# Kernel optimization log

Measured on AMD Instinct MI355X. Metric: run time of the kernel, lower is better.

Reference implementation:

```python
import jax, jax.numpy as jnp
import numpy as np

N_SITES = 100000
GRID = 192
C_IN = 256
C_MID = 64
C_OUT = 256


def _build_neighbor_idx(rng):
    # unique active voxel coordinates in a GRID^3 volume
    flat = rng.choice(GRID ** 3, size=N_SITES, replace=False).astype(np.int64)
    coords = np.stack(np.unravel_index(flat, (GRID, GRID, GRID)), axis=1)  # [N,3]
    order = np.argsort(flat)
    flat_sorted = flat[order]
    offs = np.array([(dx, dy, dz) for dx in (-1, 0, 1) for dy in (-1, 0, 1) for dz in (-1, 0, 1)], dtype=np.int64)  # [27,3]
    nb = np.full((N_SITES, 27), N_SITES, dtype=np.int64)  # N_SITES = "missing" pad row
    for k in range(27):
        nc = coords + offs[k]
        valid = np.all((nc >= 0) & (nc < GRID), axis=1)
        nflat = nc[:, 0] * GRID * GRID + nc[:, 1] * GRID + nc[:, 2]
        pos = np.searchsorted(flat_sorted, nflat)
        pos_c = np.clip(pos, 0, N_SITES - 1)
        found = valid & (flat_sorted[pos_c] == nflat)
        nb[:, k] = np.where(found, order[pos_c], N_SITES)
    return nb


def setup_inputs() -> dict:
    key = jax.random.key(0)
    ks = jax.random.split(key, 8)
    rng = np.random.default_rng(0)
    neighbor_idx = jnp.asarray(_build_neighbor_idx(rng))  # [N,27] int
    features = jax.random.normal(ks[0], (N_SITES, C_IN), dtype=jnp.float32)
    # conv weights (scn convs have no bias here)
    W1 = jax.random.normal(ks[1], (C_IN, C_MID), dtype=jnp.float32) * 0.02   # 1x1x1 submanifold conv
    W2 = jax.random.normal(ks[2], (27, C_MID, C_MID), dtype=jnp.float32) * 0.02  # 3x3x3 submanifold conv
    W3 = jax.random.normal(ks[3], (C_MID, C_OUT), dtype=jnp.float32) * 0.02  # 1x1x1 submanifold conv
    # SparseAffineChannel3d: weight ~ U[0,1), bias = 0
    g1 = jax.random.uniform(ks[4], (C_MID,), dtype=jnp.float32)
    b1 = jnp.zeros((C_MID,), dtype=jnp.float32)
    g2 = jax.random.uniform(ks[5], (C_MID,), dtype=jnp.float32)
    b2 = jnp.zeros((C_MID,), dtype=jnp.float32)
    g3 = jax.random.uniform(ks[6], (C_OUT,), dtype=jnp.float32)
    b3 = jnp.zeros((C_OUT,), dtype=jnp.float32)
    return {"features": features, "W1": W1, "W2": W2, "W3": W3,
            "g1": g1, "b1": b1, "g2": g2, "b2": b2, "g3": g3, "b3": b3,
            "neighbor_idx": neighbor_idx}


def _submanifold_conv3(h, W2, neighbor_idx):
    # gather-GEMM: missing neighbors (index N_SITES) read the zero pad row
    h_pad = jnp.concatenate([h, jnp.zeros((1, h.shape[1]), dtype=h.dtype)], axis=0)
    gathered = h_pad[neighbor_idx]  # [N, 27, C_MID]
    return jnp.einsum('nkc,kcd->nd', gathered, W2)


def reference(features, W1, W2, W3, g1, b1, g2, b2, g3, b3, neighbor_idx):
    residual = features
    # conv1 (1x1x1 submanifold) + affine + relu
    out = features @ W1
    out = jax.nn.relu(out * g1 + b1)
    # conv2 (3x3x3 submanifold) + affine + relu
    out = _submanifold_conv3(out, W2, neighbor_idx)
    out = jax.nn.relu(out * g2 + b2)
    # conv3 (1x1x1 submanifold) + affine
    out = out @ W3
    out = out * g3 + b3
    # residual add + relu
    return jax.nn.relu(out + residual)
```

## Files before the change

kernel.cpp:

```cpp
#include <hip/hip_runtime.h>

#define N_SITES 100000
#define C_IN 256
#define C_MID 64
#define C_OUT 256

typedef __attribute__((ext_vector_type(8))) short bf16x8;
typedef __attribute__((ext_vector_type(4))) float f32x4;

__device__ inline short f2bf(float f) {
  unsigned u = __builtin_bit_cast(unsigned, f);
  u += 0x7fffu + ((u >> 16) & 1u);
  return (short)(u >> 16);
}

__device__ inline f32x4 mfma16(bf16x8 a, bf16x8 b, f32x4 c) {
  return __builtin_amdgcn_mfma_f32_16x16x32_bf16(a, b, c, 0, 0, 0);
}

__global__ __launch_bounds__(256) void k_prep(const float* __restrict__ W1,
                                              const float* __restrict__ W2,
                                              const float* __restrict__ W3,
                                              short* __restrict__ W1T,
                                              short* __restrict__ W2T,
                                              short* __restrict__ W3T,
                                              short* __restrict__ h1) {
  int i = blockIdx.x * 256 + threadIdx.x;
  if (i < 16384) {
    int n = i >> 8, k = i & 255;
    W1T[i] = f2bf(W1[k * 64 + n]);
  } else if (i < 16384 + 110592) {
    int j = i - 16384;
    int k = j >> 12, rem = j & 4095;
    int dout = rem >> 6, din = rem & 63;
    W2T[j] = f2bf(W2[k * 4096 + din * 64 + dout]);
  } else if (i < 16384 + 110592 + 16384) {
    int j = i - (16384 + 110592);
    int n = j >> 6, k = j & 63;
    W3T[j] = f2bf(W3[k * 256 + n]);
  } else if (i < 16384 + 110592 + 16384 + 64) {
    h1[(size_t)N_SITES * 64 + (i - (16384 + 110592 + 16384))] = 0;
  }
}

__global__ __launch_bounds__(256) void k_conv1(const float* __restrict__ F,
                                               const short* __restrict__ W1T,
                                               const float* __restrict__ g1,
                                               const float* __restrict__ b1,
                                               short* __restrict__ h1) {
  int tid = threadIdx.x;
  int lane = tid & 63, wave = tid >> 6;
  int l15 = lane & 15, l4 = lane >> 4;
  int base = blockIdx.x * 64 + wave * 16;

  int row = base + l15;
  int rowc = row < N_SITES ? row : (N_SITES - 1);
  const float* fr = F + (size_t)rowc * 256 + l4 * 8;

  f32x4 acc[4];
#pragma unroll
  for (int nf = 0; nf < 4; ++nf) acc[nf] = (f32x4){0.f, 0.f, 0.f, 0.f};

#pragma unroll
  for (int kk = 0; kk < 8; ++kk) {
    float4 a0 = *(const float4*)(fr + kk * 32);
    float4 a1 = *(const float4*)(fr + kk * 32 + 4);
    bf16x8 af;
    af[0] = f2bf(a0.x); af[1] = f2bf(a0.y); af[2] = f2bf(a0.z); af[3] = f2bf(a0.w);
    af[4] = f2bf(a1.x); af[5] = f2bf(a1.y); af[6] = f2bf(a1.z); af[7] = f2bf(a1.w);
#pragma unroll
    for (int nf = 0; nf < 4; ++nf) {
      bf16x8 bf = *(const bf16x8*)(W1T + (nf * 16 + l15) * 256 + kk * 32 + l4 * 8);
      acc[nf] = mfma16(af, bf, acc[nf]);
    }
  }

#pragma unroll
  for (int nf = 0; nf < 4; ++nf) {
    int col = nf * 16 + l15;
    float g = g1[col], bb = b1[col];
#pragma unroll
    for (int r = 0; r < 4; ++r) {
      int site = base + l4 * 4 + r;
      if (site < N_SITES) {
        float v = fmaxf(acc[nf][r] * g + bb, 0.f);
        h1[(size_t)site * 64 + col] = f2bf(v);
      }
    }
  }
}

__global__ __launch_bounds__(256) void k_conv2(const short* __restrict__ h1,
                                               const short* __restrict__ W2T,
                                               const float* __restrict__ g2,
                                               const float* __restrict__ b2,
                                               const int* __restrict__ NB,
                                               short* __restrict__ h2) {
  __shared__ int nbt[128 * 27];
  int tid = threadIdx.x;
  int blockbase = blockIdx.x * 128;
  for (int i = tid; i < 128 * 27; i += 256) {
    int site = blockbase + i / 27;
    nbt[i] = (site < N_SITES) ? NB[(size_t)site * 27 + (i % 27)] : N_SITES;
  }
  __syncthreads();

  int lane = tid & 63, wave = tid >> 6;
  int l15 = lane & 15, l4 = lane >> 4;
  int rowl0 = wave * 32 + l15;
  int rowl1 = wave * 32 + 16 + l15;

  f32x4 acc[2][4];
#pragma unroll
  for (int mf = 0; mf < 2; ++mf)
#pragma unroll
    for (int nf = 0; nf < 4; ++nf) acc[mf][nf] = (f32x4){0.f, 0.f, 0.f, 0.f};

  for (int k = 0; k < 27; ++k) {
    int n0 = nbt[rowl0 * 27 + k];
    int n1 = nbt[rowl1 * 27 + k];
    const short* p0 = h1 + (size_t)n0 * 64 + l4 * 8;
    const short* p1 = h1 + (size_t)n1 * 64 + l4 * 8;
#pragma unroll
    for (int kkk = 0; kkk < 2; ++kkk) {
      bf16x8 a0 = *(const bf16x8*)(p0 + kkk * 32);
      bf16x8 a1 = *(const bf16x8*)(p1 + kkk * 32);
#pragma unroll
      for (int nf = 0; nf < 4; ++nf) {
        bf16x8 bfr = *(const bf16x8*)(W2T + (k * 64 + nf * 16 + l15) * 64 + kkk * 32 + l4 * 8);
        acc[0][nf] = mfma16(a0, bfr, acc[0][nf]);
        acc[1][nf] = mfma16(a1, bfr, acc[1][nf]);
      }
    }
  }

#pragma unroll
  for (int mf = 0; mf < 2; ++mf) {
#pragma unroll
    for (int nf = 0; nf < 4; ++nf) {
      int col = nf * 16 + l15;
      float g = g2[col], bb = b2[col];
#pragma unroll
      for (int r = 0; r < 4; ++r) {
        int site = blockbase + wave * 32 + mf * 16 + l4 * 4 + r;
        if (site < N_SITES) {
          float v = fmaxf(acc[mf][nf][r] * g + bb, 0.f);
          h2[(size_t)site * 64 + col] = f2bf(v);
        }
      }
    }
  }
}

__global__ __launch_bounds__(256) void k_conv3(const short* __restrict__ h2,
                                               const short* __restrict__ W3T,
                                               const float* __restrict__ g3,
                                               const float* __restrict__ b3,
                                               const float* __restrict__ F,
                                               float* __restrict__ out) {
  int tid = threadIdx.x;
  int lane = tid & 63, wave = tid >> 6;
  int l15 = lane & 15, l4 = lane >> 4;
  int base = blockIdx.x * 32;

  const short* pa0 = h2 + (size_t)(base + l15) * 64 + l4 * 8;
  const short* pa1 = h2 + (size_t)(base + 16 + l15) * 64 + l4 * 8;

  f32x4 acc[2][4];
#pragma unroll
  for (int mf = 0; mf < 2; ++mf)
#pragma unroll
    for (int nf = 0; nf < 4; ++nf) acc[mf][nf] = (f32x4){0.f, 0.f, 0.f, 0.f};

#pragma unroll
  for (int kkk = 0; kkk < 2; ++kkk) {
    bf16x8 a0 = *(const bf16x8*)(pa0 + kkk * 32);
    bf16x8 a1 = *(const bf16x8*)(pa1 + kkk * 32);
#pragma unroll
    for (int nf = 0; nf < 4; ++nf) {
      bf16x8 b = *(const bf16x8*)(W3T + (wave * 64 + nf * 16 + l15) * 64 + kkk * 32 + l4 * 8);
      acc[0][nf] = mfma16(a0, b, acc[0][nf]);
      acc[1][nf] = mfma16(a1, b, acc[1][nf]);
    }
  }

#pragma unroll
  for (int mf = 0; mf < 2; ++mf) {
#pragma unroll
    for (int nf = 0; nf < 4; ++nf) {
      int col = wave * 64 + nf * 16 + l15;
      float g = g3[col], bb = b3[col];
#pragma unroll
      for (int r = 0; r < 4; ++r) {
        int site = base + mf * 16 + l4 * 4 + r;
        size_t o = (size_t)site * 256 + col;
        float v = acc[mf][nf][r] * g + bb + F[o];
        out[o] = fmaxf(v, 0.f);
      }
    }
  }
}

extern "C" void kernel_launch(void* const* d_in, const int* in_sizes, int n_in,
                              void* d_out, int out_size, void* d_ws, size_t ws_size,
                              hipStream_t stream) {
  const float* F  = (const float*)d_in[0];
  const float* W1 = (const float*)d_in[1];
  const float* W2 = (const float*)d_in[2];
  const float* W3 = (const float*)d_in[3];
  const float* g1 = (const float*)d_in[4];
  const float* b1 = (const float*)d_in[5];
  const float* g2 = (const float*)d_in[6];
  const float* b2 = (const float*)d_in[7];
  const float* g3 = (const float*)d_in[8];
  const float* b3 = (const float*)d_in[9];
  const int*   NB = (const int*)d_in[10];
  float* out = (float*)d_out;

  char* ws = (char*)d_ws;
  short* W1T = (short*)(ws);
  short* W2T = (short*)(ws + 32768);
  short* W3T = (short*)(ws + 32768 + 221184);
  short* h1  = (short*)(ws + 32768 + 221184 + 32768);
  short* h2  = (short*)(ws + 32768 + 221184 + 32768 + 12800128);

  k_prep<<<dim3(561), dim3(256), 0, stream>>>(W1, W2, W3, W1T, W2T, W3T, h1);
  k_conv1<<<dim3((N_SITES + 63) / 64), dim3(256), 0, stream>>>(F, W1T, g1, b1, h1);
  k_conv2<<<dim3((N_SITES + 127) / 128), dim3(256), 0, stream>>>(h1, W2T, g2, b2, NB, h2);
  k_conv3<<<dim3(N_SITES / 32), dim3(256), 0, stream>>>(h2, W3T, g3, b3, F, out);
}
```

Baseline: 365.7 us.

## Restructure conv kernels: prefetch gathers, swap conv3 operands, vectorize stores

conv1 now issues all of its feature loads before doing any math. conv2 gives each wave 16 sites in 64-site blocks and prefetches the next neighbor row to overlap the gather latency. conv3 swaps the MFMA operands so each lane holds 4 consecutive output channels, which allows float4 residual loads and float4 output stores; each wave covers 16 sites across all 256 channels. Launch bounds with occupancy hints are added and the bf16 conversion now uses the library intrinsic. The cost is more registers per thread (16 accumulators in conv3) and, in conv2, less reuse of W2 loads across sites.

```diff
diff --git a/kernel.cpp b/kernel.cpp
--- a/kernel.cpp
+++ b/kernel.cpp
@@ -1,4 +1,5 @@
 #include <hip/hip_runtime.h>
+#include <hip/hip_bf16.h>
 
 #define N_SITES 100000
 #define C_IN 256
@@ -9,9 +10,7 @@
 typedef __attribute__((ext_vector_type(4))) float f32x4;
 
 __device__ inline short f2bf(float f) {
-  unsigned u = __builtin_bit_cast(unsigned, f);
-  u += 0x7fffu + ((u >> 16) & 1u);
-  return (short)(u >> 16);
+  return __builtin_bit_cast(short, __float2bfloat16(f));
 }
 
 __device__ inline f32x4 mfma16(bf16x8 a, bf16x8 b, f32x4 c) {
@@ -43,11 +42,11 @@
   }
 }
 
-__global__ __launch_bounds__(256) void k_conv1(const float* __restrict__ F,
-                                               const short* __restrict__ W1T,
-                                               const float* __restrict__ g1,
-                                               const float* __restrict__ b1,
-                                               short* __restrict__ h1) {
+__global__ __launch_bounds__(256, 4) void k_conv1(const float* __restrict__ F,
+                                                  const short* __restrict__ W1T,
+                                                  const float* __restrict__ g1,
+                                                  const float* __restrict__ b1,
+                                                  short* __restrict__ h1) {
   int tid = threadIdx.x;
   int lane = tid & 63, wave = tid >> 6;
   int l15 = lane & 15, l4 = lane >> 4;
@@ -57,14 +56,20 @@
   int rowc = row < N_SITES ? row : (N_SITES - 1);
   const float* fr = F + (size_t)rowc * 256 + l4 * 8;
 
+  float4 fa[16];
+#pragma unroll
+  for (int kk = 0; kk < 8; ++kk) {
+    fa[2 * kk]     = *(const float4*)(fr + kk * 32);
+    fa[2 * kk + 1] = *(const float4*)(fr + kk * 32 + 4);
+  }
+
   f32x4 acc[4];
 #pragma unroll
   for (int nf = 0; nf < 4; ++nf) acc[nf] = (f32x4){0.f, 0.f, 0.f, 0.f};
 
 #pragma unroll
   for (int kk = 0; kk < 8; ++kk) {
-    float4 a0 = *(const float4*)(fr + kk * 32);
-    float4 a1 = *(const float4*)(fr + kk * 32 + 4);
+    float4 a0 = fa[2 * kk], a1 = fa[2 * kk + 1];
     bf16x8 af;
     af[0] = f2bf(a0.x); af[1] = f2bf(a0.y); af[2] = f2bf(a0.z); af[3] = f2bf(a0.w);
     af[4] = f2bf(a1.x); af[5] = f2bf(a1.y); af[6] = f2bf(a1.z); af[7] = f2bf(a1.w);
@@ -90,16 +95,16 @@
   }
 }
 
-__global__ __launch_bounds__(256) void k_conv2(const short* __restrict__ h1,
-                                               const short* __restrict__ W2T,
-                                               const float* __restrict__ g2,
-                                               const float* __restrict__ b2,
-                                               const int* __restrict__ NB,
-                                               short* __restrict__ h2) {
-  __shared__ int nbt[128 * 27];
+__global__ __launch_bounds__(256, 6) void k_conv2(const short* __restrict__ h1,
+                                                  const short* __restrict__ W2T,
+                                                  const float* __restrict__ g2,
+                                                  const float* __restrict__ b2,
+                                                  const int* __restrict__ NB,
+                                                  short* __restrict__ h2) {
+  __shared__ int nbt[64 * 27];
   int tid = threadIdx.x;
-  int blockbase = blockIdx.x * 128;
-  for (int i = tid; i < 128 * 27; i += 256) {
+  int blockbase = blockIdx.x * 64;
+  for (int i = tid; i < 64 * 27; i += 256) {
     int site = blockbase + i / 27;
     nbt[i] = (site < N_SITES) ? NB[(size_t)site * 27 + (i % 27)] : N_SITES;
   }
@@ -107,96 +112,96 @@
 
   int lane = tid & 63, wave = tid >> 6;
   int l15 = lane & 15, l4 = lane >> 4;
-  int rowl0 = wave * 32 + l15;
-  int rowl1 = wave * 32 + 16 + l15;
-
-  f32x4 acc[2][4];
-#pragma unroll
-  for (int mf = 0; mf < 2; ++mf)
-#pragma unroll
-    for (int nf = 0; nf < 4; ++nf) acc[mf][nf] = (f32x4){0.f, 0.f, 0.f, 0.f};
+  const int* myNb = nbt + (wave * 16 + l15) * 27;
+  const short* wbase = W2T + l15 * 64 + l4 * 8;
+
+  f32x4 acc[4];
+#pragma unroll
+  for (int nf = 0; nf < 4; ++nf) acc[nf] = (f32x4){0.f, 0.f, 0.f, 0.f};
+
+  int n0 = myNb[0];
+  const short* p = h1 + (size_t)n0 * 64 + l4 * 8;
+  bf16x8 a0 = *(const bf16x8*)p;
+  bf16x8 a1 = *(const bf16x8*)(p + 32);
 
   for (int k = 0; k < 27; ++k) {
-    int n0 = nbt[rowl0 * 27 + k];
-    int n1 = nbt[rowl1 * 27 + k];
-    const short* p0 = h1 + (size_t)n0 * 64 + l4 * 8;
-    const short* p1 = h1 + (size_t)n1 * 64 + l4 * 8;
-#pragma unroll
-    for (int kkk = 0; kkk < 2; ++kkk) {
-      bf16x8 a0 = *(const bf16x8*)(p0 + kkk * 32);
-      bf16x8 a1 = *(const bf16x8*)(p1 + kkk * 32);
-#pragma unroll
-      for (int nf = 0; nf < 4; ++nf) {
-        bf16x8 bfr = *(const bf16x8*)(W2T + (k * 64 + nf * 16 + l15) * 64 + kkk * 32 + l4 * 8);
-        acc[0][nf] = mfma16(a0, bfr, acc[0][nf]);
-        acc[1][nf] = mfma16(a1, bfr, acc[1][nf]);
+    int kn = k < 26 ? k + 1 : 26;
+    int n = myNb[kn];
+    const short* q = h1 + (size_t)n * 64 + l4 * 8;
+    bf16x8 na0 = *(const bf16x8*)q;
+    bf16x8 na1 = *(const bf16x8*)(q + 32);
+
+    const short* wk = wbase + k * 4096;
+#pragma unroll
+    for (int nf = 0; nf < 4; ++nf) {
+      bf16x8 b0 = *(const bf16x8*)(wk + nf * 1024);
+      bf16x8 b1 = *(const bf16x8*)(wk + nf * 1024 + 32);
+      acc[nf] = mfma16(a0, b0, acc[nf]);
+      acc[nf] = mfma16(a1, b1, acc[nf]);
+    }
+    a0 = na0;
+    a1 = na1;
+  }
+
+#pragma unroll
+  for (int nf = 0; nf < 4; ++nf) {
+    int col = nf * 16 + l15;
+    float g = g2[col], bb = b2[col];
+#pragma unroll
+    for (int r = 0; r < 4; ++r) {
+      int site = blockbase + wave * 16 + l4 * 4 + r;
+      if (site < N_SITES) {
+        float v = fmaxf(acc[nf][r] * g + bb, 0.f);
+        h2[(size_t)site * 64 + col] = f2bf(v);
       }
     }
   }
-
-#pragma unroll
-  for (int mf = 0; mf < 2; ++mf) {
-#pragma unroll
-    for (int nf = 0; nf < 4; ++nf) {
-      int col = nf * 16 + l15;
-      float g = g2[col], bb = b2[col];
-#pragma unroll
-      for (int r = 0; r < 4; ++r) {
-        int site = blockbase + wave * 32 + mf * 16 + l4 * 4 + r;
-        if (site < N_SITES) {
-          float v = fmaxf(acc[mf][nf][r] * g + bb, 0.f);
-          h2[(size_t)site * 64 + col] = f2bf(v);
-        }
-      }
-    }
-  }
-}
-
-__global__ __launch_bounds__(256) void k_conv3(const short* __restrict__ h2,
-                                               const short* __restrict__ W3T,
-                                               const float* __restrict__ g3,
-                                               const float* __restrict__ b3,
-                                               const float* __restrict__ F,
-                                               float* __restrict__ out) {
+}
+
+__global__ __launch_bounds__(256, 4) void k_conv3(const short* __restrict__ h2,
+                                                  const short* __restrict__ W3T,
+                                                  const float* __restrict__ g3,
+                                                  const float* __restrict__ b3,
+                                                  const float* __restrict__ F,
+                                                  float* __restrict__ out) {
   int tid = threadIdx.x;
   int lane = tid & 63, wave = tid >> 6;
   int l15 = lane & 15, l4 = lane >> 4;
-  int base = blockIdx.x * 32;
-
-  const short* pa0 = h2 + (size_t)(base + l15) * 64 + l4 * 8;
-  const short* pa1 = h2 + (size_t)(base + 16 + l15) * 64 + l4 * 8;
-
-  f32x4 acc[2][4];
-#pragma unroll
-  for (int mf = 0; mf < 2; ++mf)
-#pragma unroll
-    for (int nf = 0; nf < 4; ++nf) acc[mf][nf] = (f32x4){0.f, 0.f, 0.f, 0.f};
-
-#pragma unroll
-  for (int kkk = 0; kkk < 2; ++kkk) {
-    bf16x8 a0 = *(const bf16x8*)(pa0 + kkk * 32);
-    bf16x8 a1 = *(const bf16x8*)(pa1 + kkk * 32);
-#pragma unroll
-    for (int nf = 0; nf < 4; ++nf) {
-      bf16x8 b = *(const bf16x8*)(W3T + (wave * 64 + nf * 16 + l15) * 64 + kkk * 32 + l4 * 8);
-      acc[0][nf] = mfma16(a0, b, acc[0][nf]);
-      acc[1][nf] = mfma16(a1, b, acc[1][nf]);
-    }
-  }
-
-#pragma unroll
-  for (int mf = 0; mf < 2; ++mf) {
-#pragma unroll
-    for (int nf = 0; nf < 4; ++nf) {
-      int col = wave * 64 + nf * 16 + l15;
-      float g = g3[col], bb = b3[col];
-#pragma unroll
-      for (int r = 0; r < 4; ++r) {
-        int site = base + mf * 16 + l4 * 4 + r;
-        size_t o = (size_t)site * 256 + col;
-        float v = acc[mf][nf][r] * g + bb + F[o];
-        out[o] = fmaxf(v, 0.f);
-      }
+  int sbase = blockIdx.x * 64 + wave * 16;
+
+  int site = sbase + l15;
+  int sitec = site < N_SITES ? site : (N_SITES - 1);
+  const short* pb = h2 + (size_t)sitec * 64 + l4 * 8;
+  bf16x8 bv0 = *(const bf16x8*)pb;
+  bf16x8 bv1 = *(const bf16x8*)(pb + 32);
+
+  f32x4 acc[16];
+#pragma unroll
+  for (int nb = 0; nb < 16; ++nb) acc[nb] = (f32x4){0.f, 0.f, 0.f, 0.f};
+
+#pragma unroll
+  for (int nb = 0; nb < 16; ++nb) {
+    const short* pa = W3T + (nb * 16 + l15) * 64 + l4 * 8;
+    bf16x8 a0 = *(const bf16x8*)pa;
+    bf16x8 a1 = *(const bf16x8*)(pa + 32);
+    acc[nb] = mfma16(a0, bv0, acc[nb]);
+    acc[nb] = mfma16(a1, bv1, acc[nb]);
+  }
+
+  if (site < N_SITES) {
+#pragma unroll
+    for (int nb = 0; nb < 16; ++nb) {
+      int chan = nb * 16 + l4 * 4;
+      size_t o = (size_t)site * 256 + chan;
+      float4 g = *(const float4*)(g3 + chan);
+      float4 bb = *(const float4*)(b3 + chan);
+      float4 fv = *(const float4*)(F + o);
+      float4 r;
+      r.x = fmaxf(acc[nb][0] * g.x + bb.x + fv.x, 0.f);
+      r.y = fmaxf(acc[nb][1] * g.y + bb.y + fv.y, 0.f);
+      r.z = fmaxf(acc[nb][2] * g.z + bb.z + fv.z, 0.f);
+      r.w = fmaxf(acc[nb][3] * g.w + bb.w + fv.w, 0.f);
+      *(float4*)(out + o) = r;
     }
   }
 }
@@ -226,6 +231,6 @@
 
   k_prep<<<dim3(561), dim3(256), 0, stream>>>(W1, W2, W3, W1T, W2T, W3T, h1);
   k_conv1<<<dim3((N_SITES + 63) / 64), dim3(256), 0, stream>>>(F, W1T, g1, b1, h1);
-  k_conv2<<<dim3((N_SITES + 127) / 128), dim3(256), 0, stream>>>(h1, W2T, g2, b2, NB, h2);
-  k_conv3<<<dim3(N_SITES / 32), dim3(256), 0, stream>>>(h2, W3T, g3, b3, F, out);
-}
+  k_conv2<<<dim3((N_SITES + 63) / 64), dim3(256), 0, stream>>>(h1, W2T, g2, b2, NB, h2);
+  k_conv3<<<dim3((N_SITES + 63) / 64), dim3(256), 0, stream>>>(h2, W3T, g3, b3, F, out);
+}
```

Result: slower. 452.8 us (+23.8%).
